# Kernel optimization log

Measured on AMD Instinct MI355X. Metric: run time of the kernel, lower is better.

## Reference

```python
import jax, jax.numpy as jnp
import numpy as np

N_NODES = 50000
N_EDGES = 600000
F_IN = 128
HID = 128
LN_EPS = 1e-5


def setup_inputs() -> dict:
    key = jax.random.key(0)
    ks = jax.random.split(key, 8)
    x = jax.random.normal(ks[0], (N_NODES, F_IN), dtype=jnp.float32)
    edge_index = jax.random.randint(ks[1], (2, N_EDGES), 0, N_NODES, dtype=jnp.int64)
    s1 = 1.0 / np.sqrt(F_IN)
    s2 = 1.0 / np.sqrt(HID)
    return {
        "x": x,
        "edge_index": edge_index,
        "W1": jax.random.normal(ks[2], (F_IN, HID), dtype=jnp.float32) * s1,
        "b1": jnp.zeros((HID,), dtype=jnp.float32),
        "g1": jnp.ones((HID,), dtype=jnp.float32),
        "be1": jnp.zeros((HID,), dtype=jnp.float32),
        "W2": jax.random.normal(ks[3], (HID, HID), dtype=jnp.float32) * s2,
        "b2": jnp.zeros((HID,), dtype=jnp.float32),
        "g2": jnp.ones((HID,), dtype=jnp.float32),
        "be2": jnp.zeros((HID,), dtype=jnp.float32),
    }


def _layer_norm(h, g, b):
    mu = jnp.mean(h, axis=-1, keepdims=True)
    var = jnp.mean(jnp.square(h - mu), axis=-1, keepdims=True)
    return (h - mu) * jax.lax.rsqrt(var + LN_EPS) * g + b


def reference(x, edge_index, W1, b1, g1, be1, W2, b2, g2, be2):
    n = x.shape[0]
    src, dst = edge_index[0], edge_index[1]
    # GCN symmetric normalization with self-loops: deg = in-degree(A) + 1
    deg = jax.ops.segment_sum(jnp.ones_like(src, dtype=x.dtype), dst, num_segments=n) + 1.0
    dinv = jax.lax.rsqrt(deg)                       # D^{-1/2}, [N]
    enorm = (dinv[src] * dinv[dst])[:, None]        # per-edge norm, [E,1]
    self_norm = (dinv * dinv)[:, None]              # self-loop norm,  [N,1]

    def gcn(h, W, b):
        h = h @ W                                   # [N,HID]
        agg = jax.ops.segment_sum(h[src] * enorm, dst, num_segments=n)
        return agg + h * self_norm + b

    h = jax.nn.relu(_layer_norm(gcn(x, W1, b1), g1, be1))
    h = jax.nn.relu(_layer_norm(gcn(h, W2, b2), g2, be2))
    return h  # dropout is identity in eval; LSTM evolution only runs in training
```

## Files before the change

kernel.cpp:

```cpp
#include <hip/hip_runtime.h>

#define N_NODES 50000
#define N_EDGES 600000
#define HID 128
#define LN_EPS 1e-5f
#define MAXDEG 64
#define NB_GEMM1 782
#define NB_PLACE 2344

typedef __attribute__((ext_vector_type(8))) short short8;
typedef __attribute__((ext_vector_type(4))) float f32x4;

__device__ inline float b2f(unsigned short u) {
    union { unsigned int i; float f; } v;
    v.i = ((unsigned int)u) << 16;
    return v.f;
}
__device__ inline unsigned short f2b(float f) {
    union { float f; unsigned int u; } v; v.f = f;
    unsigned int r = (v.u + 0x7FFFu + ((v.u >> 16) & 1u)) >> 16;
    return (unsigned short)r;
}

__global__ __launch_bounds__(256) void k_prep(const float* __restrict__ W1,
                                              const float* __restrict__ W2,
                                              unsigned short* __restrict__ WT1,
                                              unsigned short* __restrict__ WT2,
                                              int* __restrict__ cursor) {
    const int bid = blockIdx.x, tid = threadIdx.x;
    if (bid < 64) {
        const int i = bid * 256 + tid;
        WT1[(i & 127) * 128 + (i >> 7)] = f2b(W1[i]);
    } else if (bid < 128) {
        const int i = (bid - 64) * 256 + tid;
        WT2[(i & 127) * 128 + (i >> 7)] = f2b(W2[i]);
    } else {
        const int i = (bid - 128) * 256 + tid;
        if (i < N_NODES) cursor[i] = 0;
    }
}

__global__ __launch_bounds__(256) void k_fused1(const float* __restrict__ x,
                                                const unsigned short* __restrict__ WT1,
                                                const int* __restrict__ ei,
                                                int* __restrict__ cursor,
                                                int* __restrict__ esrc,
                                                unsigned short* __restrict__ hb) {
    const int tid = threadIdx.x;

    if (blockIdx.x >= NB_GEMM1) {
        const int e = (blockIdx.x - NB_GEMM1) * 256 + tid;
        if (e < N_EDGES) {
            const int d = ei[N_EDGES + e];
            const int pos = atomicAdd(&cursor[d], 1);
            if (pos < MAXDEG) esrc[d * MAXDEG + pos] = ei[e];
        }
        return;
    }

    const int lane = tid & 63;
    const int ln   = lane & 15;
    const int quad = lane >> 4;
    const int m0   = blockIdx.x * 64 + (tid >> 6) * 16;

    f32x4 acc[8];
#pragma unroll
    for (int t = 0; t < 8; ++t) acc[t] = (f32x4){0.f, 0.f, 0.f, 0.f};

    int arow = m0 + ln;
    if (arow >= N_NODES) arow = N_NODES - 1;
    const float* aptr = x + (size_t)arow * HID + quad * 8;
    const unsigned short* bptr = WT1 + (size_t)ln * HID + quad * 8;

#pragma unroll
    for (int ks = 0; ks < 4; ++ks) {
        const float4 v0 = *(const float4*)(aptr + ks * 32);
        const float4 v1 = *(const float4*)(aptr + ks * 32 + 4);
        short8 a;
        a[0] = (short)f2b(v0.x); a[1] = (short)f2b(v0.y);
        a[2] = (short)f2b(v0.z); a[3] = (short)f2b(v0.w);
        a[4] = (short)f2b(v1.x); a[5] = (short)f2b(v1.y);
        a[6] = (short)f2b(v1.z); a[7] = (short)f2b(v1.w);
#pragma unroll
        for (int t = 0; t < 8; ++t) {
            const short8 b = *(const short8*)(bptr + (size_t)t * 16 * HID + ks * 32);
            acc[t] = __builtin_amdgcn_mfma_f32_16x16x32_bf16(a, b, acc[t], 0, 0, 0);
        }
    }

#pragma unroll
    for (int t = 0; t < 8; ++t) {
#pragma unroll
        for (int r = 0; r < 4; ++r) {
            const int row = m0 + quad * 4 + r;
            if (row < N_NODES) hb[(size_t)row * HID + t * 16 + ln] = f2b(acc[t][r]);
        }
    }
}

template <bool FUSE>
__device__ __forceinline__ void agg_body(const int* __restrict__ cursor,
                                         const int* __restrict__ esrc,
                                         const unsigned short* __restrict__ h,
                                         const float* __restrict__ bia,
                                         const float* __restrict__ g,
                                         const float* __restrict__ be,
                                         const unsigned short* __restrict__ WT2,
                                         unsigned short* __restrict__ hb2,
                                         float* __restrict__ outf) {
    __shared__ float pbuf[2048];
    const int tid  = threadIdx.x;
    const int wv   = tid >> 6;
    const int lane = tid & 63;
    const int grp  = lane >> 4;
    const int fl   = lane & 15;
    const int half = wv >> 2;
    const int r    = (wv & 3) * 4 + grp;
    const int row  = blockIdx.x * 16 + r;

    const int cntA  = cursor[row];
    const int cnt   = cntA < MAXDEG ? cntA : MAXDEG;
    const int ebase = row * MAXDEG;
    const int c0    = ((cnt + 7) >> 3) << 2;
    const int h0n   = c0 < cnt ? c0 : cnt;
    const int eb    = half ? ebase + h0n : ebase;
    const int ee    = half ? ebase + cnt : ebase + h0n;

    float acc[8];
#pragma unroll
    for (int j = 0; j < 8; ++j) acc[j] = 0.f;

    int e = eb;
    for (; e + 3 < ee; e += 4) {
        const int4 s4 = *(const int4*)(esrc + e);
        const short8 v0 = *(const short8*)(h + (size_t)s4.x * HID + 8 * fl);
        const short8 v1 = *(const short8*)(h + (size_t)s4.y * HID + 8 * fl);
        const short8 v2 = *(const short8*)(h + (size_t)s4.z * HID + 8 * fl);
        const short8 v3 = *(const short8*)(h + (size_t)s4.w * HID + 8 * fl);
        if constexpr (FUSE) {
            const float w0 = rsqrtf((float)cursor[s4.x] + 1.0f);
            const float w1 = rsqrtf((float)cursor[s4.y] + 1.0f);
            const float w2 = rsqrtf((float)cursor[s4.z] + 1.0f);
            const float w3 = rsqrtf((float)cursor[s4.w] + 1.0f);
#pragma unroll
            for (int j = 0; j < 8; ++j) {
                acc[j] = fmaf(w0, b2f((unsigned short)v0[j]), acc[j]);
                acc[j] = fmaf(w1, b2f((unsigned short)v1[j]), acc[j]);
                acc[j] = fmaf(w2, b2f((unsigned short)v2[j]), acc[j]);
                acc[j] = fmaf(w3, b2f((unsigned short)v3[j]), acc[j]);
            }
        } else {
#pragma unroll
            for (int j = 0; j < 8; ++j) {
                acc[j] += b2f((unsigned short)v0[j]) + b2f((unsigned short)v1[j]);
                acc[j] += b2f((unsigned short)v2[j]) + b2f((unsigned short)v3[j]);
            }
        }
    }
    for (; e < ee; ++e) {
        const int sA = esrc[e];
        const short8 vA = *(const short8*)(h + (size_t)sA * HID + 8 * fl);
        float wA = 1.0f;
        if constexpr (FUSE) wA = rsqrtf((float)cursor[sA] + 1.0f);
#pragma unroll
        for (int j = 0; j < 8; ++j)
            acc[j] = fmaf(wA, b2f((unsigned short)vA[j]), acc[j]);
    }

    if (half == 1) {
#pragma unroll
        for (int j = 0; j < 8; ++j) pbuf[r * 128 + 8 * fl + j] = acc[j];
    }
    __syncthreads();

    float o[8];
    if (half == 0) {
#pragma unroll
        for (int j = 0; j < 8; ++j) acc[j] += pbuf[r * 128 + 8 * fl + j];

        const float dd = rsqrtf((float)cntA + 1.0f);
        const short8 hv = *(const short8*)(h + (size_t)row * HID + 8 * fl);
        const float4 b0 = *(const float4*)(bia + 8 * fl);
        const float4 b1 = *(const float4*)(bia + 8 * fl + 4);
        const float bb[8] = {b0.x, b0.y, b0.z, b0.w, b1.x, b1.y, b1.z, b1.w};

        float v[8], s = 0.f, ss = 0.f;
#pragma unroll
        for (int j = 0; j < 8; ++j) {
            if constexpr (FUSE) {
                const float sn = dd * dd;
                v[j] = dd * acc[j] + b2f((unsigned short)hv[j]) * sn + bb[j];
            } else {
                v[j] = dd * (acc[j] + b2f((unsigned short)hv[j])) + bb[j];
            }
            s += v[j];
            ss = fmaf(v[j], v[j], ss);
        }
#pragma unroll
        for (int off = 1; off <= 8; off <<= 1) {
            s  += __shfl_xor(s, off);
            ss += __shfl_xor(ss, off);
        }
        const float mu  = s * (1.0f / 128.0f);
        const float var = ss * (1.0f / 128.0f) - mu * mu;
        const float rs  = rsqrtf(var + LN_EPS);

        const float4 g0  = *(const float4*)(g + 8 * fl);
        const float4 g1  = *(const float4*)(g + 8 * fl + 4);
        const float4 e0v = *(const float4*)(be + 8 * fl);
        const float4 e1v = *(const float4*)(be + 8 * fl + 4);
        const float gg[8] = {g0.x, g0.y, g0.z, g0.w, g1.x, g1.y, g1.z, g1.w};
        const float ee2[8] = {e0v.x, e0v.y, e0v.z, e0v.w, e1v.x, e1v.y, e1v.z, e1v.w};
#pragma unroll
        for (int j = 0; j < 8; ++j)
            o[j] = fmaxf((v[j] - mu) * rs * gg[j] + ee2[j], 0.0f);
    }

    if constexpr (!FUSE) {
        if (half == 0) {
            float4 w0 = {o[0], o[1], o[2], o[3]};
            float4 w1 = {o[4], o[5], o[6], o[7]};
            *(float4*)(outf + (size_t)row * HID + 8 * fl) = w0;
            *(float4*)(outf + (size_t)row * HID + 8 * fl + 4) = w1;
        }
    } else {
        __syncthreads();
        unsigned short* tile = (unsigned short*)pbuf;
        if (half == 0) {
            short8 w;
#pragma unroll
            for (int j = 0; j < 8; ++j) w[j] = (short)f2b(o[j]);
            *(short8*)&tile[r * 128 + ((8 * fl) ^ ((r & 7) << 3))] = w;
        }
        __syncthreads();

        f32x4 c = (f32x4){0.f, 0.f, 0.f, 0.f};
        const int n0 = wv * 16 + fl;
#pragma unroll
        for (int ks = 0; ks < 4; ++ks) {
            const short8 a  = *(const short8*)&tile[fl * 128 + ((grp * 8 + ks * 32) ^ ((fl & 7) << 3))];
            const short8 bf = *(const short8*)(WT2 + (size_t)n0 * HID + grp * 8 + ks * 32);
            c = __builtin_amdgcn_mfma_f32_16x16x32_bf16(a, bf, c, 0, 0, 0);
        }
#pragma unroll
        for (int rr = 0; rr < 4; ++rr) {
            const int orow = blockIdx.x * 16 + grp * 4 + rr;
            const float sc = rsqrtf((float)cursor[orow] + 1.0f);
            hb2[(size_t)orow * HID + n0] = f2b(c[rr] * sc);
        }
    }
}

__global__ __launch_bounds__(512, 4) void k_agg_fuse(const int* __restrict__ cursor,
                                                     const int* __restrict__ esrc,
                                                     const unsigned short* __restrict__ h,
                                                     const float* __restrict__ bia,
                                                     const float* __restrict__ g,
                                                     const float* __restrict__ be,
                                                     const unsigned short* __restrict__ WT2,
                                                     unsigned short* __restrict__ hb2) {
    agg_body<true>(cursor, esrc, h, bia, g, be, WT2, hb2, nullptr);
}

__global__ __launch_bounds__(512, 4) void k_agg_out(const int* __restrict__ cursor,
                                                    const int* __restrict__ esrc,
                                                    const unsigned short* __restrict__ h,
                                                    const float* __restrict__ bia,
                                                    const float* __restrict__ g,
                                                    const float* __restrict__ be,
                                                    float* __restrict__ outf) {
    agg_body<false>(cursor, esrc, h, bia, g, be, nullptr, nullptr, outf);
}

extern "C" void kernel_launch(void* const* d_in, const int* in_sizes, int n_in,
                              void* d_out, int out_size, void* d_ws, size_t ws_size,
                              hipStream_t stream) {
    (void)in_sizes; (void)n_in; (void)out_size; (void)ws_size;

    const float* x   = (const float*)d_in[0];
    const int*   ei  = (const int*)d_in[1];
    const float* W1  = (const float*)d_in[2];
    const float* b1  = (const float*)d_in[3];
    const float* g1  = (const float*)d_in[4];
    const float* be1 = (const float*)d_in[5];
    const float* W2  = (const float*)d_in[6];
    const float* b2  = (const float*)d_in[7];
    const float* g2  = (const float*)d_in[8];
    const float* be2 = (const float*)d_in[9];
    float* out = (float*)d_out;

    int* cursor = (int*)d_ws;
    int* esrc   = (int*)d_ws + 50016;
    unsigned short* WT1 = (unsigned short*)((int*)d_ws + 3250016);
    unsigned short* WT2 = (unsigned short*)((int*)d_ws + 3258208);
    unsigned short* hb  = (unsigned short*)((int*)d_ws + 3266400);
    unsigned short* hb2 = (unsigned short*)((int*)d_ws + 6466400);

    k_prep<<<324, 256, 0, stream>>>(W1, W2, WT1, WT2, cursor);
    k_fused1<<<NB_GEMM1 + NB_PLACE, 256, 0, stream>>>(x, WT1, ei, cursor, esrc, hb);

    k_agg_fuse<<<N_NODES / 16, 512, 0, stream>>>(cursor, esrc, hb, b1, g1, be1, WT2, hb2);
    k_agg_out<<<N_NODES / 16, 512, 0, stream>>>(cursor, esrc, hb2, b2, g2, be2, out);
}
```

Measured before the change: 213.8 us.

## Merge GEMM, edge placement and both aggregations into one persistent-style kernel

Replaces the three launches after prep with a single kernel whose blocks are partitioned into phases (GEMM1, edge placement, layer-1 aggregation, layer-2 aggregation), synchronised by global atomic phase counters with spin-waiting. It also splits GEMM1 into half-N tiles with WT1 staged in swizzled LDS, and drops the two-half edge split in aggregation so each 256-thread block handles 16 rows alone. This is meant to remove launch gaps and tail effects between stages. It relies on blocks being dispatched in index order, since waiting blocks spin while earlier-indexed producers must still make progress.

```diff
diff --git a/kernel.cpp b/kernel.cpp
--- a/kernel.cpp
+++ b/kernel.cpp
@@ -5,8 +5,10 @@
 #define HID 128
 #define LN_EPS 1e-5f
 #define MAXDEG 64
-#define NB_GEMM1 782
+#define NB_GEMM 1564
 #define NB_PLACE 2344
+#define NB_AGG 3125
+#define PH1_TARGET (NB_GEMM + NB_PLACE)
 
 typedef __attribute__((ext_vector_type(8))) short short8;
 typedef __attribute__((ext_vector_type(4))) float f32x4;
@@ -22,11 +24,26 @@
     return (unsigned short)r;
 }
 
+__device__ inline void ph_signal(int* ph) {
+    __syncthreads();
+    if (threadIdx.x == 0) {
+        __threadfence();
+        atomicAdd(ph, 1);
+    }
+}
+__device__ inline void ph_wait(int* ph, int target) {
+    if (threadIdx.x == 0) {
+        while (atomicAdd(ph, 0) < target) __builtin_amdgcn_s_sleep(16);
+        __threadfence();
+    }
+    __syncthreads();
+}
+
 __global__ __launch_bounds__(256) void k_prep(const float* __restrict__ W1,
                                               const float* __restrict__ W2,
                                               unsigned short* __restrict__ WT1,
                                               unsigned short* __restrict__ WT2,
-                                              int* __restrict__ cursor) {
+                                              int* __restrict__ zbase) {
     const int bid = blockIdx.x, tid = threadIdx.x;
     if (bid < 64) {
         const int i = bid * 256 + tid;
@@ -36,70 +53,13 @@
         WT2[(i & 127) * 128 + (i >> 7)] = f2b(W2[i]);
     } else {
         const int i = (bid - 128) * 256 + tid;
-        if (i < N_NODES) cursor[i] = 0;
-    }
-}
-
-__global__ __launch_bounds__(256) void k_fused1(const float* __restrict__ x,
-                                                const unsigned short* __restrict__ WT1,
-                                                const int* __restrict__ ei,
-                                                int* __restrict__ cursor,
-                                                int* __restrict__ esrc,
-                                                unsigned short* __restrict__ hb) {
-    const int tid = threadIdx.x;
-
-    if (blockIdx.x >= NB_GEMM1) {
-        const int e = (blockIdx.x - NB_GEMM1) * 256 + tid;
-        if (e < N_EDGES) {
-            const int d = ei[N_EDGES + e];
-            const int pos = atomicAdd(&cursor[d], 1);
-            if (pos < MAXDEG) esrc[d * MAXDEG + pos] = ei[e];
-        }
-        return;
-    }
-
-    const int lane = tid & 63;
-    const int ln   = lane & 15;
-    const int quad = lane >> 4;
-    const int m0   = blockIdx.x * 64 + (tid >> 6) * 16;
-
-    f32x4 acc[8];
-#pragma unroll
-    for (int t = 0; t < 8; ++t) acc[t] = (f32x4){0.f, 0.f, 0.f, 0.f};
-
-    int arow = m0 + ln;
-    if (arow >= N_NODES) arow = N_NODES - 1;
-    const float* aptr = x + (size_t)arow * HID + quad * 8;
-    const unsigned short* bptr = WT1 + (size_t)ln * HID + quad * 8;
-
-#pragma unroll
-    for (int ks = 0; ks < 4; ++ks) {
-        const float4 v0 = *(const float4*)(aptr + ks * 32);
-        const float4 v1 = *(const float4*)(aptr + ks * 32 + 4);
-        short8 a;
-        a[0] = (short)f2b(v0.x); a[1] = (short)f2b(v0.y);
-        a[2] = (short)f2b(v0.z); a[3] = (short)f2b(v0.w);
-        a[4] = (short)f2b(v1.x); a[5] = (short)f2b(v1.y);
-        a[6] = (short)f2b(v1.z); a[7] = (short)f2b(v1.w);
-#pragma unroll
-        for (int t = 0; t < 8; ++t) {
-            const short8 b = *(const short8*)(bptr + (size_t)t * 16 * HID + ks * 32);
-            acc[t] = __builtin_amdgcn_mfma_f32_16x16x32_bf16(a, b, acc[t], 0, 0, 0);
-        }
-    }
-
-#pragma unroll
-    for (int t = 0; t < 8; ++t) {
-#pragma unroll
-        for (int r = 0; r < 4; ++r) {
-            const int row = m0 + quad * 4 + r;
-            if (row < N_NODES) hb[(size_t)row * HID + t * 16 + ln] = f2b(acc[t][r]);
-        }
+        if (i < N_NODES + 2) zbase[i] = 0;
     }
 }
 
 template <bool FUSE>
-__device__ __forceinline__ void agg_body(const int* __restrict__ cursor,
+__device__ __forceinline__ void agg_tile(const int tileid, const int tid,
+                                         const int* __restrict__ cursor,
                                          const int* __restrict__ esrc,
                                          const unsigned short* __restrict__ h,
                                          const float* __restrict__ bia,
@@ -107,31 +67,26 @@
                                          const float* __restrict__ be,
                                          const unsigned short* __restrict__ WT2,
                                          unsigned short* __restrict__ hb2,
-                                         float* __restrict__ outf) {
-    __shared__ float pbuf[2048];
-    const int tid  = threadIdx.x;
+                                         float* __restrict__ outf,
+                                         unsigned short* smem) {
     const int wv   = tid >> 6;
     const int lane = tid & 63;
     const int grp  = lane >> 4;
     const int fl   = lane & 15;
-    const int half = wv >> 2;
-    const int r    = (wv & 3) * 4 + grp;
-    const int row  = blockIdx.x * 16 + r;
+    const int r    = wv * 4 + grp;
+    const int row  = tileid * 16 + r;
 
     const int cntA  = cursor[row];
     const int cnt   = cntA < MAXDEG ? cntA : MAXDEG;
     const int ebase = row * MAXDEG;
-    const int c0    = ((cnt + 7) >> 3) << 2;
-    const int h0n   = c0 < cnt ? c0 : cnt;
-    const int eb    = half ? ebase + h0n : ebase;
-    const int ee    = half ? ebase + cnt : ebase + h0n;
+    const int e1    = ebase + cnt;
 
     float acc[8];
 #pragma unroll
     for (int j = 0; j < 8; ++j) acc[j] = 0.f;
 
-    int e = eb;
-    for (; e + 3 < ee; e += 4) {
+    int e = ebase;
+    for (; e + 3 < e1; e += 4) {
         const int4 s4 = *(const int4*)(esrc + e);
         const short8 v0 = *(const short8*)(h + (size_t)s4.x * HID + 8 * fl);
         const short8 v1 = *(const short8*)(h + (size_t)s4.y * HID + 8 * fl);
@@ -157,7 +112,7 @@
             }
         }
     }
-    for (; e < ee; ++e) {
+    for (; e < e1; ++e) {
         const int sA = esrc[e];
         const short8 vA = *(const short8*)(h + (size_t)sA * HID + 8 * fl);
         float wA = 1.0f;
@@ -167,109 +122,169 @@
             acc[j] = fmaf(wA, b2f((unsigned short)vA[j]), acc[j]);
     }
 
-    if (half == 1) {
-#pragma unroll
-        for (int j = 0; j < 8; ++j) pbuf[r * 128 + 8 * fl + j] = acc[j];
-    }
-    __syncthreads();
-
+    const float dd = rsqrtf((float)cntA + 1.0f);
+    const short8 hv = *(const short8*)(h + (size_t)row * HID + 8 * fl);
+    const float4 b0 = *(const float4*)(bia + 8 * fl);
+    const float4 b1 = *(const float4*)(bia + 8 * fl + 4);
+    const float bb[8] = {b0.x, b0.y, b0.z, b0.w, b1.x, b1.y, b1.z, b1.w};
+
+    float v[8], s = 0.f, ss = 0.f;
+#pragma unroll
+    for (int j = 0; j < 8; ++j) {
+        if constexpr (FUSE) {
+            const float sn = dd * dd;
+            v[j] = dd * acc[j] + b2f((unsigned short)hv[j]) * sn + bb[j];
+        } else {
+            v[j] = dd * (acc[j] + b2f((unsigned short)hv[j])) + bb[j];
+        }
+        s += v[j];
+        ss = fmaf(v[j], v[j], ss);
+    }
+#pragma unroll
+    for (int off = 1; off <= 8; off <<= 1) {
+        s  += __shfl_xor(s, off);
+        ss += __shfl_xor(ss, off);
+    }
+    const float mu  = s * (1.0f / 128.0f);
+    const float var = ss * (1.0f / 128.0f) - mu * mu;
+    const float rs  = rsqrtf(var + LN_EPS);
+
+    const float4 g0  = *(const float4*)(g + 8 * fl);
+    const float4 g1  = *(const float4*)(g + 8 * fl + 4);
+    const float4 e0v = *(const float4*)(be + 8 * fl);
+    const float4 e1v = *(const float4*)(be + 8 * fl + 4);
+    const float gg[8] = {g0.x, g0.y, g0.z, g0.w, g1.x, g1.y, g1.z, g1.w};
+    const float ee2[8] = {e0v.x, e0v.y, e0v.z, e0v.w, e1v.x, e1v.y, e1v.z, e1v.w};
     float o[8];
-    if (half == 0) {
-#pragma unroll
-        for (int j = 0; j < 8; ++j) acc[j] += pbuf[r * 128 + 8 * fl + j];
-
-        const float dd = rsqrtf((float)cntA + 1.0f);
-        const short8 hv = *(const short8*)(h + (size_t)row * HID + 8 * fl);
-        const float4 b0 = *(const float4*)(bia + 8 * fl);
-        const float4 b1 = *(const float4*)(bia + 8 * fl + 4);
-        const float bb[8] = {b0.x, b0.y, b0.z, b0.w, b1.x, b1.y, b1.z, b1.w};
-
-        float v[8], s = 0.f, ss = 0.f;
-#pragma unroll
-        for (int j = 0; j < 8; ++j) {
-            if constexpr (FUSE) {
-                const float sn = dd * dd;
-                v[j] = dd * acc[j] + b2f((unsigned short)hv[j]) * sn + bb[j];
-            } else {
-                v[j] = dd * (acc[j] + b2f((unsigned short)hv[j])) + bb[j];
-            }
-            s += v[j];
-            ss = fmaf(v[j], v[j], ss);
-        }
-#pragma unroll
-        for (int off = 1; off <= 8; off <<= 1) {
-            s  += __shfl_xor(s, off);
-            ss += __shfl_xor(ss, off);
-        }
-        const float mu  = s * (1.0f / 128.0f);
-        const float var = ss * (1.0f / 128.0f) - mu * mu;
-        const float rs  = rsqrtf(var + LN_EPS);
-
-        const float4 g0  = *(const float4*)(g + 8 * fl);
-        const float4 g1  = *(const float4*)(g + 8 * fl + 4);
-        const float4 e0v = *(const float4*)(be + 8 * fl);
-        const float4 e1v = *(const float4*)(be + 8 * fl + 4);
-        const float gg[8] = {g0.x, g0.y, g0.z, g0.w, g1.x, g1.y, g1.z, g1.w};
-        const float ee2[8] = {e0v.x, e0v.y, e0v.z, e0v.w, e1v.x, e1v.y, e1v.z, e1v.w};
-#pragma unroll
-        for (int j = 0; j < 8; ++j)
-            o[j] = fmaxf((v[j] - mu) * rs * gg[j] + ee2[j], 0.0f);
-    }
+#pragma unroll
+    for (int j = 0; j < 8; ++j)
+        o[j] = fmaxf((v[j] - mu) * rs * gg[j] + ee2[j], 0.0f);
 
     if constexpr (!FUSE) {
-        if (half == 0) {
-            float4 w0 = {o[0], o[1], o[2], o[3]};
-            float4 w1 = {o[4], o[5], o[6], o[7]};
-            *(float4*)(outf + (size_t)row * HID + 8 * fl) = w0;
-            *(float4*)(outf + (size_t)row * HID + 8 * fl + 4) = w1;
-        }
+        float4 w0 = {o[0], o[1], o[2], o[3]};
+        float4 w1 = {o[4], o[5], o[6], o[7]};
+        *(float4*)(outf + (size_t)row * HID + 8 * fl) = w0;
+        *(float4*)(outf + (size_t)row * HID + 8 * fl + 4) = w1;
     } else {
+        short8 w;
+#pragma unroll
+        for (int j = 0; j < 8; ++j) w[j] = (short)f2b(o[j]);
+        *(short8*)&smem[r * 128 + ((8 * fl) ^ ((r & 7) << 3))] = w;
         __syncthreads();
-        unsigned short* tile = (unsigned short*)pbuf;
-        if (half == 0) {
-            short8 w;
-#pragma unroll
-            for (int j = 0; j < 8; ++j) w[j] = (short)f2b(o[j]);
-            *(short8*)&tile[r * 128 + ((8 * fl) ^ ((r & 7) << 3))] = w;
+
+        f32x4 c0 = (f32x4){0.f, 0.f, 0.f, 0.f};
+        f32x4 c1 = (f32x4){0.f, 0.f, 0.f, 0.f};
+        const int n0 = wv * 32 + fl;
+#pragma unroll
+        for (int ks = 0; ks < 4; ++ks) {
+            const short8 a   = *(const short8*)&smem[fl * 128 + ((grp * 8 + ks * 32) ^ ((fl & 7) << 3))];
+            const short8 bf0 = *(const short8*)(WT2 + (size_t)n0 * HID + grp * 8 + ks * 32);
+            c0 = __builtin_amdgcn_mfma_f32_16x16x32_bf16(a, bf0, c0, 0, 0, 0);
+            const short8 bf1 = *(const short8*)(WT2 + (size_t)(n0 + 16) * HID + grp * 8 + ks * 32);
+            c1 = __builtin_amdgcn_mfma_f32_16x16x32_bf16(a, bf1, c1, 0, 0, 0);
+        }
+#pragma unroll
+        for (int rr = 0; rr < 4; ++rr) {
+            const int orow = tileid * 16 + grp * 4 + rr;
+            const float sc = rsqrtf((float)cursor[orow] + 1.0f);
+            hb2[(size_t)orow * HID + n0]      = f2b(c0[rr] * sc);
+            hb2[(size_t)orow * HID + n0 + 16] = f2b(c1[rr] * sc);
+        }
+    }
+}
+
+__global__ __launch_bounds__(256) void k_main(
+        const float* __restrict__ x, const int* __restrict__ ei,
+        const unsigned short* __restrict__ WT1, const unsigned short* __restrict__ WT2,
+        const float* __restrict__ b1, const float* __restrict__ g1, const float* __restrict__ be1,
+        const float* __restrict__ b2, const float* __restrict__ g2, const float* __restrict__ be2,
+        int* __restrict__ cursor, int* ph1, int* ph2,
+        int* __restrict__ esrc,
+        unsigned short* __restrict__ hb, unsigned short* __restrict__ hb2,
+        float* __restrict__ out) {
+    __shared__ unsigned short smem[8192];
+    const int tid = threadIdx.x;
+    int bid = blockIdx.x;
+
+    if (bid < NB_GEMM) {
+        const int mt = bid >> 1, nh = bid & 1;
+        {
+            const short8* src8 = (const short8*)(WT1 + nh * 64 * HID);
+#pragma unroll
+            for (int it = 0; it < 4; ++it) {
+                const int c  = it * 256 + tid;
+                const int nn = c >> 4;
+                const int kc = (c & 15) ^ (nn & 7);
+                ((short8*)smem)[c] = src8[nn * 16 + kc];
+            }
         }
         __syncthreads();
 
-        f32x4 c = (f32x4){0.f, 0.f, 0.f, 0.f};
-        const int n0 = wv * 16 + fl;
+        const int lane = tid & 63;
+        const int ln   = lane & 15;
+        const int quad = lane >> 4;
+        const int m0   = mt * 64 + (tid >> 6) * 16;
+
+        f32x4 acc[4];
+#pragma unroll
+        for (int t = 0; t < 4; ++t) acc[t] = (f32x4){0.f, 0.f, 0.f, 0.f};
+
+        int arow = m0 + ln;
+        if (arow >= N_NODES) arow = N_NODES - 1;
+        const float* aptr = x + (size_t)arow * HID + quad * 8;
+
 #pragma unroll
         for (int ks = 0; ks < 4; ++ks) {
-            const short8 a  = *(const short8*)&tile[fl * 128 + ((grp * 8 + ks * 32) ^ ((fl & 7) << 3))];
-            const short8 bf = *(const short8*)(WT2 + (size_t)n0 * HID + grp * 8 + ks * 32);
-            c = __builtin_amdgcn_mfma_f32_16x16x32_bf16(a, bf, c, 0, 0, 0);
-        }
-#pragma unroll
-        for (int rr = 0; rr < 4; ++rr) {
-            const int orow = blockIdx.x * 16 + grp * 4 + rr;
-            const float sc = rsqrtf((float)cursor[orow] + 1.0f);
-            hb2[(size_t)orow * HID + n0] = f2b(c[rr] * sc);
-        }
-    }
-}
-
-__global__ __launch_bounds__(512, 4) void k_agg_fuse(const int* __restrict__ cursor,
-                                                     const int* __restrict__ esrc,
-                                                     const unsigned short* __restrict__ h,
-                                                     const float* __restrict__ bia,
-                                                     const float* __restrict__ g,
-                                                     const float* __restrict__ be,
-                                                     const unsigned short* __restrict__ WT2,
-                                                     unsigned short* __restrict__ hb2) {
-    agg_body<true>(cursor, esrc, h, bia, g, be, WT2, hb2, nullptr);
-}
-
-__global__ __launch_bounds__(512, 4) void k_agg_out(const int* __restrict__ cursor,
-                                                    const int* __restrict__ esrc,
-                                                    const unsigned short* __restrict__ h,
-                                                    const float* __restrict__ bia,
-                                                    const float* __restrict__ g,
-                                                    const float* __restrict__ be,
-                                                    float* __restrict__ outf) {
-    agg_body<false>(cursor, esrc, h, bia, g, be, nullptr, nullptr, outf);
+            const float4 v0 = *(const float4*)(aptr + ks * 32);
+            const float4 v1 = *(const float4*)(aptr + ks * 32 + 4);
+            short8 a;
+            a[0] = (short)f2b(v0.x); a[1] = (short)f2b(v0.y);
+            a[2] = (short)f2b(v0.z); a[3] = (short)f2b(v0.w);
+            a[4] = (short)f2b(v1.x); a[5] = (short)f2b(v1.y);
+            a[6] = (short)f2b(v1.z); a[7] = (short)f2b(v1.w);
+#pragma unroll
+            for (int t = 0; t < 4; ++t) {
+                const int nn = t * 16 + ln;
+                const short8 b = *(const short8*)&smem[nn * 128 + ((quad * 8 + ks * 32) ^ ((nn & 7) << 3))];
+                acc[t] = __builtin_amdgcn_mfma_f32_16x16x32_bf16(a, b, acc[t], 0, 0, 0);
+            }
+        }
+
+#pragma unroll
+        for (int t = 0; t < 4; ++t) {
+#pragma unroll
+            for (int rr = 0; rr < 4; ++rr) {
+                const int row = m0 + quad * 4 + rr;
+                if (row < N_NODES) hb[(size_t)row * HID + nh * 64 + t * 16 + ln] = f2b(acc[t][rr]);
+            }
+        }
+        ph_signal(ph1);
+        return;
+    }
+    bid -= NB_GEMM;
+
+    if (bid < NB_PLACE) {
+        const int e = bid * 256 + tid;
+        if (e < N_EDGES) {
+            const int d = ei[N_EDGES + e];
+            const int pos = atomicAdd(&cursor[d], 1);
+            if (pos < MAXDEG) esrc[d * MAXDEG + pos] = ei[e];
+        }
+        ph_signal(ph1);
+        return;
+    }
+    bid -= NB_PLACE;
+
+    if (bid < NB_AGG) {
+        ph_wait(ph1, PH1_TARGET);
+        agg_tile<true>(bid, tid, cursor, esrc, hb, b1, g1, be1, WT2, hb2, nullptr, smem);
+        ph_signal(ph2);
+        return;
+    }
+    bid -= NB_AGG;
+
+    ph_wait(ph2, NB_AGG);
+    agg_tile<false>(bid, tid, cursor, esrc, hb2, b2, g2, be2, nullptr, nullptr, out, smem);
 }
 
 extern "C" void kernel_launch(void* const* d_in, const int* in_sizes, int n_in,
@@ -290,15 +305,16 @@
     float* out = (float*)d_out;
 
     int* cursor = (int*)d_ws;
+    int* ph1    = cursor + N_NODES;
+    int* ph2    = cursor + N_NODES + 1;
     int* esrc   = (int*)d_ws + 50016;
     unsigned short* WT1 = (unsigned short*)((int*)d_ws + 3250016);
     unsigned short* WT2 = (unsigned short*)((int*)d_ws + 3258208);
     unsigned short* hb  = (unsigned short*)((int*)d_ws + 3266400);
     unsigned short* hb2 = (unsigned short*)((int*)d_ws + 6466400);
 
-    k_prep<<<324, 256, 0, stream>>>(W1, W2, WT1, WT2, cursor);
-    k_fused1<<<NB_GEMM1 + NB_PLACE, 256, 0, stream>>>(x, WT1, ei, cursor, esrc, hb);
-
-    k_agg_fuse<<<N_NODES / 16, 512, 0, stream>>>(cursor, esrc, hb, b1, g1, be1, WT2, hb2);
-    k_agg_out<<<N_NODES / 16, 512, 0, stream>>>(cursor, esrc, hb2, b2, g2, be2, out);
-}
+    k_prep<<<325, 256, 0, stream>>>(W1, W2, WT1, WT2, cursor);
+    k_main<<<NB_GEMM + NB_PLACE + 2 * NB_AGG, 256, 0, stream>>>(
+        x, ei, WT1, WT2, b1, g1, be1, b2, g2, be2,
+        cursor, ph1, ph2, esrc, hb, hb2, out);
+}
```

Measured after the change: 771.4 us. 261% more time.
